# Kernel tuning notes

Hardware: AMD Instinct MI355X
Metric: run time of the kernel (lower is better)

Reference implementation:

```python
import jax, jax.numpy as jnp
import numpy as np

IN_F = 8192
OUT_F = 8192
M = 32  # tokens (small -> memory-bound dequant+GEMV-like)


def setup_inputs() -> dict:
    key = jax.random.key(0)
    k1, k2, k3 = jax.random.split(key, 3)
    x = jax.random.normal(k1, (M, IN_F), dtype=jnp.float32)
    # int8-range quantized weights, stored as int8 like the torch buffer
    weight_quantized = jax.random.randint(k2, (OUT_F, IN_F), -128, 128, dtype=jnp.int32).astype(jnp.int8)
    # positive per-output-channel scales (clamped min 1e-8 in quantize())
    weight_scale = jax.random.uniform(k3, (OUT_F,), dtype=jnp.float32) * 0.02 + 1e-8
    return {"x": x, "weight_quantized": weight_quantized, "weight_scale": weight_scale}


def reference(x, weight_quantized, weight_scale):
    # dequantize: W[o,i] = int8[o,i] * scale[o]  (full fp32 materialization, as in source)
    w = weight_quantized.astype(jnp.float32) * weight_scale[:, None]  # [OUT_F, IN_F]
    # F.linear: x @ W^T
    return jnp.einsum('mi,oi->mo', x, w)
```

## Files before the change

### kernel.cpp

```cpp
#include <hip/hip_runtime.h>
#include <stdint.h>

#define IN_F   8192
#define OUT_F  8192
#define M_TOK  32
#define BN     16
#define BK     128
#define NIT    (IN_F / BK)
#define PF     2
#define LDSS   136

typedef float  f32x4  __attribute__((ext_vector_type(4)));
typedef short  short8 __attribute__((ext_vector_type(8)));

#define LDS_BARRIER() do {                                   \
    asm volatile("s_waitcnt lgkmcnt(0)" ::: "memory");       \
    __builtin_amdgcn_s_barrier();                            \
} while (0)

__device__ inline unsigned pk_bf16(float f0, float f1) {
    unsigned u0 = __builtin_bit_cast(unsigned, f0);
    unsigned u1 = __builtin_bit_cast(unsigned, f1);
    return (u0 >> 16) | (u1 & 0xFFFF0000u);
}

__global__ __launch_bounds__(256, 2) void qlin_mfma(
    const float* __restrict__ x, const int* __restrict__ wq,
    const float* __restrict__ scale, float* __restrict__ out) {

    __shared__ ushort ldsA[2][M_TOK][LDSS];
    __shared__ ushort ldsW[2][BN][LDSS];
    __shared__ f32x4  red[2][64];

    const int t  = threadIdx.x;
    const int o0 = blockIdx.x * BN;

    const int ra  = t >> 3;
    const int ca  = (t & 7) * 16;
    const int rw  = t >> 4;
    const int cw  = (t & 15) * 8;

    const float* xp = x  + (size_t)ra * IN_F + ca;
    const int*   wp = wq + (size_t)(o0 + rw) * IN_F + cw;

    float4 abuf[PF][4];
    int4   wbuf[PF][2];

    #pragma unroll
    for (int p = 0; p < PF; ++p) {
        #pragma unroll
        for (int q = 0; q < 4; ++q)
            abuf[p][q] = *reinterpret_cast<const float4*>(xp + p * BK + 4 * q);
        wbuf[p][0] = *reinterpret_cast<const int4*>(wp + p * BK);
        wbuf[p][1] = *reinterpret_cast<const int4*>(wp + p * BK + 4);
    }

    const int wid  = t >> 6;
    const int lane = t & 63;
    const int mt   = wid & 1;
    const int kh   = wid >> 1;
    const int frow = lane & 15;
    const int fk   = (lane >> 4) * 8;

    f32x4 acc = {0.f, 0.f, 0.f, 0.f};

    for (int base = 0; base < NIT; base += PF) {
        #pragma unroll
        for (int p = 0; p < PF; ++p) {
            const int it  = base + p;
            const int buf = it & 1;

            {
                float4 v0 = abuf[p][0], v1 = abuf[p][1];
                float4 v2 = abuf[p][2], v3 = abuf[p][3];
                uint4 w0, w1;
                w0.x = pk_bf16(v0.x, v0.y); w0.y = pk_bf16(v0.z, v0.w);
                w0.z = pk_bf16(v1.x, v1.y); w0.w = pk_bf16(v1.z, v1.w);
                w1.x = pk_bf16(v2.x, v2.y); w1.y = pk_bf16(v2.z, v2.w);
                w1.z = pk_bf16(v3.x, v3.y); w1.w = pk_bf16(v3.z, v3.w);
                *reinterpret_cast<uint4*>(&ldsA[buf][ra][ca])     = w0;
                *reinterpret_cast<uint4*>(&ldsA[buf][ra][ca + 8]) = w1;
            }
            {
                int4 a0 = wbuf[p][0], a1 = wbuf[p][1];
                uint4 w0;
                w0.x = pk_bf16((float)a0.x, (float)a0.y);
                w0.y = pk_bf16((float)a0.z, (float)a0.w);
                w0.z = pk_bf16((float)a1.x, (float)a1.y);
                w0.w = pk_bf16((float)a1.z, (float)a1.w);
                *reinterpret_cast<uint4*>(&ldsW[buf][rw][cw]) = w0;
            }

            const int nit = it + PF;
            if (nit < NIT) {
                #pragma unroll
                for (int q = 0; q < 4; ++q)
                    abuf[p][q] = *reinterpret_cast<const float4*>(xp + nit * BK + 4 * q);
                wbuf[p][0] = *reinterpret_cast<const int4*>(wp + nit * BK);
                wbuf[p][1] = *reinterpret_cast<const int4*>(wp + nit * BK + 4);
            }

            LDS_BARRIER();

            const ushort* aB = &ldsA[buf][mt * 16 + frow][kh * 64 + fk];
            const ushort* wB = &ldsW[buf][frow][kh * 64 + fk];
            #pragma unroll
            for (int ks = 0; ks < 2; ++ks) {
                short8 af = *reinterpret_cast<const short8*>(aB + ks * 32);
                short8 bf = *reinterpret_cast<const short8*>(wB + ks * 32);
                acc = __builtin_amdgcn_mfma_f32_16x16x32_bf16(af, bf, acc, 0, 0, 0);
            }
        }
    }

    if (kh == 1) red[mt][lane] = acc;
    __syncthreads();
    if (kh == 0) {
        f32x4 s = acc + red[mt][lane];
        const int   ocol = o0 + frow;
        const float sc   = scale[ocol];
        const int   m0   = mt * 16 + (lane >> 4) * 4;
        #pragma unroll
        for (int rg = 0; rg < 4; ++rg)
            out[(size_t)(m0 + rg) * OUT_F + ocol] = s[rg] * sc;
    }
}

extern "C" void kernel_launch(void* const* d_in, const int* in_sizes, int n_in,
                              void* d_out, int out_size, void* d_ws, size_t ws_size,
                              hipStream_t stream) {
    const float* x  = (const float*)d_in[0];
    const int*   wq = (const int*)d_in[1];
    const float* sc = (const float*)d_in[2];
    float* out = (float*)d_out;

    qlin_mfma<<<OUT_F / BN, 256, 0, stream>>>(x, wq, sc, out);
}
```

Measured before the change: 63.56 us.

## Pre-convert activations to bf16 in a separate kernel and widen output tile

Adds a small pre-pass kernel that converts x from fp32 to bf16 into workspace, so the main GEMV kernel loads half the activation bytes and skips per-block conversion. The main kernel now covers 32 output channels per block with 512 threads (8 waves split across M, N and K halves), halving the number of blocks and thus the redundant x reads across blocks. This costs an extra kernel launch and a workspace round trip, and leaves fewer blocks (256) to fill the GPU.

New measurement: 78.72 us. 1.24x slower.

```diff
diff --git a/kernel.cpp b/kernel.cpp
--- a/kernel.cpp
+++ b/kernel.cpp
@@ -4,7 +4,7 @@
 #define IN_F   8192
 #define OUT_F  8192
 #define M_TOK  32
-#define BN     16
+#define BN     32
 #define BK     128
 #define NIT    (IN_F / BK)
 #define PF     2
@@ -24,33 +24,46 @@
     return (u0 >> 16) | (u1 & 0xFFFF0000u);
 }
 
-__global__ __launch_bounds__(256, 2) void qlin_mfma(
-    const float* __restrict__ x, const int* __restrict__ wq,
+__global__ __launch_bounds__(256) void xconv(
+    const float* __restrict__ x, ushort* __restrict__ xb) {
+    const size_t j = (size_t)blockIdx.x * 256 + threadIdx.x;
+    const float* p = x + j * 16;
+    float4 v0 = *reinterpret_cast<const float4*>(p);
+    float4 v1 = *reinterpret_cast<const float4*>(p + 4);
+    float4 v2 = *reinterpret_cast<const float4*>(p + 8);
+    float4 v3 = *reinterpret_cast<const float4*>(p + 12);
+    uint4 w0, w1;
+    w0.x = pk_bf16(v0.x, v0.y); w0.y = pk_bf16(v0.z, v0.w);
+    w0.z = pk_bf16(v1.x, v1.y); w0.w = pk_bf16(v1.z, v1.w);
+    w1.x = pk_bf16(v2.x, v2.y); w1.y = pk_bf16(v2.z, v2.w);
+    w1.z = pk_bf16(v3.x, v3.y); w1.w = pk_bf16(v3.z, v3.w);
+    *reinterpret_cast<uint4*>(xb + j * 16)     = w0;
+    *reinterpret_cast<uint4*>(xb + j * 16 + 8) = w1;
+}
+
+__global__ __launch_bounds__(512) void qlin_mfma(
+    const ushort* __restrict__ xb, const int* __restrict__ wq,
     const float* __restrict__ scale, float* __restrict__ out) {
 
     __shared__ ushort ldsA[2][M_TOK][LDSS];
     __shared__ ushort ldsW[2][BN][LDSS];
-    __shared__ f32x4  red[2][64];
+    __shared__ f32x4  red[2][2][64];
 
     const int t  = threadIdx.x;
     const int o0 = blockIdx.x * BN;
 
-    const int ra  = t >> 3;
-    const int ca  = (t & 7) * 16;
-    const int rw  = t >> 4;
-    const int cw  = (t & 15) * 8;
+    const int r  = t >> 4;
+    const int cc = (t & 15) * 8;
 
-    const float* xp = x  + (size_t)ra * IN_F + ca;
-    const int*   wp = wq + (size_t)(o0 + rw) * IN_F + cw;
+    const ushort* xp = xb + (size_t)r * IN_F + cc;
+    const int*    wp = wq + (size_t)(o0 + r) * IN_F + cc;
 
-    float4 abuf[PF][4];
-    int4   wbuf[PF][2];
+    int4 abuf[PF];
+    int4 wbuf[PF][2];
 
     #pragma unroll
     for (int p = 0; p < PF; ++p) {
-        #pragma unroll
-        for (int q = 0; q < 4; ++q)
-            abuf[p][q] = *reinterpret_cast<const float4*>(xp + p * BK + 4 * q);
+        abuf[p]    = *reinterpret_cast<const int4*>(xp + p * BK);
         wbuf[p][0] = *reinterpret_cast<const int4*>(wp + p * BK);
         wbuf[p][1] = *reinterpret_cast<const int4*>(wp + p * BK + 4);
     }
@@ -58,7 +71,8 @@
     const int wid  = t >> 6;
     const int lane = t & 63;
     const int mt   = wid & 1;
-    const int kh   = wid >> 1;
+    const int nt   = (wid >> 1) & 1;
+    const int kh   = wid >> 2;
     const int frow = lane & 15;
     const int fk   = (lane >> 4) * 8;
 
@@ -70,17 +84,8 @@
             const int it  = base + p;
             const int buf = it & 1;
 
-            {
-                float4 v0 = abuf[p][0], v1 = abuf[p][1];
-                float4 v2 = abuf[p][2], v3 = abuf[p][3];
-                uint4 w0, w1;
-                w0.x = pk_bf16(v0.x, v0.y); w0.y = pk_bf16(v0.z, v0.w);
-                w0.z = pk_bf16(v1.x, v1.y); w0.w = pk_bf16(v1.z, v1.w);
-                w1.x = pk_bf16(v2.x, v2.y); w1.y = pk_bf16(v2.z, v2.w);
-                w1.z = pk_bf16(v3.x, v3.y); w1.w = pk_bf16(v3.z, v3.w);
-                *reinterpret_cast<uint4*>(&ldsA[buf][ra][ca])     = w0;
-                *reinterpret_cast<uint4*>(&ldsA[buf][ra][ca + 8]) = w1;
-            }
+            *reinterpret_cast<int4*>(&ldsA[buf][r][cc]) = abuf[p];
+
             {
                 int4 a0 = wbuf[p][0], a1 = wbuf[p][1];
                 uint4 w0;
@@ -88,14 +93,12 @@
                 w0.y = pk_bf16((float)a0.z, (float)a0.w);
                 w0.z = pk_bf16((float)a1.x, (float)a1.y);
                 w0.w = pk_bf16((float)a1.z, (float)a1.w);
-                *reinterpret_cast<uint4*>(&ldsW[buf][rw][cw]) = w0;
+                *reinterpret_cast<uint4*>(&ldsW[buf][r][cc]) = w0;
             }
 
             const int nit = it + PF;
             if (nit < NIT) {
-                #pragma unroll
-                for (int q = 0; q < 4; ++q)
-                    abuf[p][q] = *reinterpret_cast<const float4*>(xp + nit * BK + 4 * q);
+                abuf[p]    = *reinterpret_cast<const int4*>(xp + nit * BK);
                 wbuf[p][0] = *reinterpret_cast<const int4*>(wp + nit * BK);
                 wbuf[p][1] = *reinterpret_cast<const int4*>(wp + nit * BK + 4);
             }
@@ -103,7 +106,7 @@
             LDS_BARRIER();
 
             const ushort* aB = &ldsA[buf][mt * 16 + frow][kh * 64 + fk];
-            const ushort* wB = &ldsW[buf][frow][kh * 64 + fk];
+            const ushort* wB = &ldsW[buf][nt * 16 + frow][kh * 64 + fk];
             #pragma unroll
             for (int ks = 0; ks < 2; ++ks) {
                 short8 af = *reinterpret_cast<const short8*>(aB + ks * 32);
@@ -113,11 +116,11 @@
         }
     }
 
-    if (kh == 1) red[mt][lane] = acc;
+    if (kh == 1) red[mt][nt][lane] = acc;
     __syncthreads();
     if (kh == 0) {
-        f32x4 s = acc + red[mt][lane];
-        const int   ocol = o0 + frow;
+        f32x4 s = acc + red[mt][nt][lane];
+        const int   ocol = o0 + nt * 16 + frow;
         const float sc   = scale[ocol];
         const int   m0   = mt * 16 + (lane >> 4) * 4;
         #pragma unroll
@@ -133,6 +136,8 @@
     const int*   wq = (const int*)d_in[1];
     const float* sc = (const float*)d_in[2];
     float* out = (float*)d_out;
+    ushort* xb = (ushort*)d_ws;
 
-    qlin_mfma<<<OUT_F / BN, 256, 0, stream>>>(x, wq, sc, out);
+    xconv<<<(M_TOK * IN_F) / (256 * 16), 256, 0, stream>>>(x, xb);
+    qlin_mfma<<<OUT_F / BN, 512, 0, stream>>>(xb, wq, sc, out);
 }
```
